# Kernel optimization log

Measured on AMD Instinct MI355X. Metric: run time of the kernel, lower is better.

The kernel has to match this reference:

```python
import jax, jax.numpy as jnp
import numpy as np

N, E, C = 20000, 320000, 10000
IN, H, D = 768, 8, 64
HD = H * D
SA_H = 128


def _gat(feat, src, dst, W, al, ar, b):
    # DGL GATConv: fc -> per-node attn terms -> edge leaky_relu -> edge softmax over dst -> scatter-add -> bias -> elu
    h = (feat @ W).reshape(N, H, D)                       # [N,H,D]
    el = (h * al).sum(-1)                                 # [N,H]
    er = (h * ar).sum(-1)                                 # [N,H]
    e = jax.nn.leaky_relu(el[src] + er[dst], 0.2)         # [E,H]
    m = jax.ops.segment_max(e, dst, num_segments=N)       # [N,H]
    m = jnp.where(jnp.isfinite(m), m, 0.0)                # zero in-degree nodes
    ee = jnp.exp(e - m[dst])                              # [E,H]
    denom = jax.ops.segment_sum(ee, dst, num_segments=N)  # [N,H]
    a = ee / jnp.maximum(denom[dst], 1e-9)                # [E,H]
    out = jax.ops.segment_sum(a[:, :, None] * h[src], dst, num_segments=N)  # [N,H,D]
    return jax.nn.elu(out + b.reshape(1, H, D))


def _sem(z, w1, b1, w2):
    # SemanticAttention: per-metapath score -> softmax over metapaths -> weighted sum
    w = (jnp.tanh(z @ w1 + b1) @ w2).mean(0)              # [M,1]
    beta = jax.nn.softmax(w, axis=0)                      # [M,1]
    return (beta[None] * z).sum(1)                        # [C,HD]


def setup_inputs():
    key = jax.random.key(0)
    ks = jax.random.split(key, 32)
    inp = {}
    for i in range(3):
        inp[f"feat{i}"] = jax.random.normal(ks[i], (N, IN), jnp.float32)
        inp[f"src{i}"] = jax.random.randint(ks[3 + i], (E,), 0, N, dtype=jnp.int32)
        inp[f"dst{i}"] = jax.random.randint(ks[6 + i], (E,), 0, N, dtype=jnp.int32)
        inp[f"char{i}"] = jnp.arange(C, dtype=jnp.int32)
        inp[f"W{i}"] = jax.random.normal(ks[9 + i], (IN, HD), jnp.float32) * 0.05
        inp[f"al{i}"] = jax.random.normal(ks[12 + i], (H, D), jnp.float32) * 0.05
        inp[f"ar{i}"] = jax.random.normal(ks[15 + i], (H, D), jnp.float32) * 0.05
        inp[f"b{i}"] = jnp.zeros((HD,), jnp.float32)
    inp["sw1"] = jax.random.normal(ks[18], (HD, SA_H), jnp.float32) * 0.05
    inp["sb1"] = jnp.zeros((SA_H,), jnp.float32)
    inp["sw2"] = jax.random.normal(ks[19], (SA_H, 1), jnp.float32) * 0.05
    inp["aw1"] = jax.random.normal(ks[20], (HD, SA_H), jnp.float32) * 0.05
    inp["ab1"] = jnp.zeros((SA_H,), jnp.float32)
    inp["aw2"] = jax.random.normal(ks[21], (SA_H, 1), jnp.float32) * 0.05
    return inp


def reference(feat0, feat1, feat2, src0, src1, src2, dst0, dst1, dst2, char0, char1, char2,
              W0, W1, W2, al0, al1, al2, ar0, ar1, ar2, b0, b1, b2,
              sw1, sb1, sw2, aw1, ab1, aw2):
    h1 = _gat(feat0, src0, dst0, W0, al0, ar0, b0)        # [N,H,D]
    hh = _gat(feat2, src2, dst2, W2, al2, ar2, b2)        # [N,H,D]
    z = jnp.stack([h1[char0].reshape(C, HD), hh[char2].reshape(C, HD)], axis=1)  # [C,2,HD]
    sound = _sem(z, sw1, sb1, sw2)                        # [C,HD]
    h2 = _gat(feat1, src1, dst1, W1, al1, ar1, b1)        # [N,H,D]
    z2 = jnp.stack([sound, h2[char1].reshape(C, HD)], axis=1)  # [C,2,HD]
    sem_emb = _sem(z2, aw1, ab1, aw2).reshape(C, H, D)    # [C,H,D]
    h1 = h1.at[char0].set(sem_emb)
    h2 = h2.at[char1].set(sem_emb)
    hh = hh.at[char2].set(sem_emb)
    return sem_emb, h1.mean(1), h2.mean(1), hh.mean(1)
```

## Files before the change

kernel.cpp:

```cpp
#include <hip/hip_runtime.h>
#include <math.h>

#define NN 20000
#define NE 320000
#define CC 10000
#define KIN 768
#define NH 8
#define ND 64
#define NHD 512
#define NSA 128
#define NBKT 79

#define WTB_SZ (NHD * KIN)
#define W1TB_SZ (NSA * NHD)

typedef __attribute__((ext_vector_type(4))) float f32x4;
typedef __attribute__((ext_vector_type(8))) short s16x8;

__device__ __forceinline__ unsigned short f2bf(float f) {
  unsigned u = __float_as_uint(f);
  u += 0x7fffu + ((u >> 16) & 1u);
  return (unsigned short)(u >> 16);
}
__device__ __forceinline__ float bf2f(unsigned short s) {
  return __uint_as_float(((unsigned)s) << 16);
}
__device__ __forceinline__ float bflo(unsigned u) { return __uint_as_float(u << 16); }
__device__ __forceinline__ float bfhi(unsigned u) { return __uint_as_float(u & 0xffff0000u); }

__device__ __forceinline__ void gl_lds16(const void* g, void* l) {
  __builtin_amdgcn_global_load_lds(
      (const __attribute__((address_space(1))) unsigned int*)g,
      (__attribute__((address_space(3))) unsigned int*)l, 16, 0, 0);
}

__global__ void k_prep(const float* __restrict__ W0, const float* __restrict__ W1,
                       const float* __restrict__ W2, const float* __restrict__ sw1,
                       const float* __restrict__ aw1, unsigned short* __restrict__ wtb3,
                       unsigned short* __restrict__ w1tb2, int* __restrict__ deg3,
                       float* __restrict__ scal) {
  int i = blockIdx.x * 256 + threadIdx.x;
  if (i < 3 * WTB_SZ) {
    int g = i / WTB_SZ;
    int j = i - g * WTB_SZ;
    int n = j / KIN, k = j - n * KIN;
    const float* W = (g == 0) ? W0 : (g == 1) ? W1 : W2;
    wtb3[i] = f2bf(W[(size_t)k * NHD + n]);
    return;
  }
  i -= 3 * WTB_SZ;
  if (i < 2 * W1TB_SZ) {
    int p = i / W1TB_SZ;
    int j = i - p * W1TB_SZ;
    int n = j / NHD, k = j - n * NHD;
    const float* W = p ? aw1 : sw1;
    w1tb2[p * W1TB_SZ + n * NHD + k] = f2bf(W[(size_t)k * NSA + n]);
    return;
  }
  i -= 2 * W1TB_SZ;
  if (i < 3 * NN) { deg3[i] = 0; return; }
  i -= 3 * NN;
  if (i < 4) scal[i] = 0.f;
}

__global__ __launch_bounds__(256, 2) void k_gemm_gat(const float* __restrict__ A,
                                                     const unsigned short* __restrict__ Bt,
                                                     unsigned short* __restrict__ outb,
                                                     const float* __restrict__ al,
                                                     const float* __restrict__ ar,
                                                     float* __restrict__ el,
                                                     float* __restrict__ er) {
  __shared__ unsigned short As[128 * 32];
  __shared__ unsigned short Bs[128 * 32];
  const int bid = blockIdx.x;
  const int xcd = bid & 7, t = bid >> 3;
  const int rowblk = (t >> 2) * 8 + xcd;
  if (rowblk * 128 >= NN) return;
  const int row0 = rowblk * 128;
  const int col0 = (t & 3) * 128;
  const int tid = threadIdx.x;
  const int wv = tid >> 6, lane = tid & 63;
  const int wr = (wv >> 1) * 64, wc = (wv & 1) * 64;
  const int ci = lane & 3, rsub = lane >> 2;

  f32x4 acc[4][4] = {};

  const int l15 = lane & 15;
  const int pc = (((lane >> 4) ^ ((l15 >> 1) & 3))) * 8;

  for (int k0 = 0; k0 < KIN; k0 += 32) {
#pragma unroll
    for (int i = 0; i < 2; i++) {
      int lrow = (wv * 2 + i) * 16 + rsub;
      int kc = (ci ^ ((lrow >> 1) & 3)) << 3;
      int ga = row0 + lrow; if (ga > NN - 1) ga = NN - 1;
      const float* ap = A + (size_t)ga * KIN + k0 + kc;
      float4 f0 = ((const float4*)ap)[0];
      float4 f1 = ((const float4*)ap)[1];
      int gb = col0 + lrow;
      gl_lds16(Bt + (size_t)gb * KIN + k0 + kc, Bs + (wv * 2 + i) * 512);
      uint4 pk;
      pk.x = ((unsigned)f2bf(f0.y) << 16) | f2bf(f0.x);
      pk.y = ((unsigned)f2bf(f0.w) << 16) | f2bf(f0.z);
      pk.z = ((unsigned)f2bf(f1.y) << 16) | f2bf(f1.x);
      pk.w = ((unsigned)f2bf(f1.w) << 16) | f2bf(f1.z);
      *(uint4*)(As + (wv * 2 + i) * 512 + lane * 8) = pk;
    }
    __syncthreads();
    s16x8 af[4], bf[4];
#pragma unroll
    for (int m = 0; m < 4; m++) {
      af[m] = *(const s16x8*)(As + (wr + m * 16 + l15) * 32 + pc);
      bf[m] = *(const s16x8*)(Bs + (wc + m * 16 + l15) * 32 + pc);
    }
#pragma unroll
    for (int m = 0; m < 4; m++)
#pragma unroll
      for (int n = 0; n < 4; n++)
        acc[m][n] = __builtin_amdgcn_mfma_f32_16x16x32_bf16(af[m], bf[n], acc[m][n], 0, 0, 0);
    __syncthreads();
  }

  const int cbase = col0 + wc + l15;
  const int rq = (lane >> 4) * 4;
  const int hd = (col0 + wc) >> 6;
  float alc[4], arc[4];
#pragma unroll
  for (int n = 0; n < 4; n++) { alc[n] = al[cbase + n * 16]; arc[n] = ar[cbase + n * 16]; }

#pragma unroll
  for (int m = 0; m < 4; m++) {
#pragma unroll
    for (int r = 0; r < 4; r++) {
      int grow = row0 + wr + m * 16 + rq + r;
      float a = 0.f, b = 0.f;
#pragma unroll
      for (int n = 0; n < 4; n++) {
        float v = acc[m][n][r];
        a += v * alc[n];
        b += v * arc[n];
      }
      a += __shfl_xor(a, 1, 64); a += __shfl_xor(a, 2, 64);
      a += __shfl_xor(a, 4, 64); a += __shfl_xor(a, 8, 64);
      b += __shfl_xor(b, 1, 64); b += __shfl_xor(b, 2, 64);
      b += __shfl_xor(b, 4, 64); b += __shfl_xor(b, 8, 64);
      if (grow < NN) {
        unsigned short* dp = outb + (size_t)grow * NHD + cbase;
#pragma unroll
        for (int n = 0; n < 4; n++) dp[n * 16] = f2bf(acc[m][n][r]);
        if (l15 == 0) {
          el[(size_t)grow * NH + hd] = a;
          er[(size_t)grow * NH + hd] = b;
        }
      }
    }
  }
}

__global__ __launch_bounds__(256, 2) void k_gemm_sem(const unsigned short* __restrict__ A0,
                                                     const unsigned short* __restrict__ A1,
                                                     const unsigned short* __restrict__ Bt,
                                                     const float* __restrict__ b1,
                                                     const float* __restrict__ w2,
                                                     float* __restrict__ scal) {
  __shared__ unsigned short As[128 * 32];
  __shared__ unsigned short Bs[128 * 32];
  __shared__ float rsum[2][128];
  __shared__ float pp[2][2];
  const int M = 2 * CC;
  const int tid = threadIdx.x;
  const int wv = tid >> 6, lane = tid & 63;
  const int row0 = blockIdx.x * 128;
  const int wr = (wv >> 1) * 64, wc = (wv & 1) * 64;
  const int ci = lane & 3, rsub = lane >> 2;

  f32x4 acc[4][4] = {};

  const int l15 = lane & 15;
  const int pc = (((lane >> 4) ^ ((l15 >> 1) & 3))) * 8;

  for (int k0 = 0; k0 < NHD; k0 += 32) {
#pragma unroll
    for (int i = 0; i < 2; i++) {
      int lrow = (wv * 2 + i) * 16 + rsub;
      int kc = (ci ^ ((lrow >> 1) & 3)) << 3;
      int ga = row0 + lrow; if (ga > M - 1) ga = M - 1;
      const unsigned short* Ap = (ga < CC) ? A0 + (size_t)ga * NHD
                                           : A1 + (size_t)(ga - CC) * NHD;
      gl_lds16(Ap + k0 + kc, As + (wv * 2 + i) * 512);
      int gb = lrow;
      gl_lds16(Bt + (size_t)gb * NHD + k0 + kc, Bs + (wv * 2 + i) * 512);
    }
    __syncthreads();
    s16x8 af[4], bf[4];
#pragma unroll
    for (int m = 0; m < 4; m++) {
      af[m] = *(const s16x8*)(As + (wr + m * 16 + l15) * 32 + pc);
      bf[m] = *(const s16x8*)(Bs + (wc + m * 16 + l15) * 32 + pc);
    }
#pragma unroll
    for (int m = 0; m < 4; m++)
#pragma unroll
      for (int n = 0; n < 4; n++)
        acc[m][n] = __builtin_amdgcn_mfma_f32_16x16x32_bf16(af[m], bf[n], acc[m][n], 0, 0, 0);
    __syncthreads();
  }

  if (tid < 128) { rsum[0][tid] = 0.f; rsum[1][tid] = 0.f; }
  __syncthreads();
  const int cb = wc + l15;
  const int rq = (lane >> 4) * 4;
  float b1c[4], w2c[4];
#pragma unroll
  for (int n = 0; n < 4; n++) { b1c[n] = b1[cb + n * 16]; w2c[n] = w2[cb + n * 16]; }
#pragma unroll
  for (int m = 0; m < 4; m++) {
#pragma unroll
    for (int r = 0; r < 4; r++) {
      int rl = wr + m * 16 + rq + r;
      float s = 0.f;
#pragma unroll
      for (int n = 0; n < 4; n++) s += tanhf(acc[m][n][r] + b1c[n]) * w2c[n];
      s += __shfl_xor(s, 1, 64); s += __shfl_xor(s, 2, 64);
      s += __shfl_xor(s, 4, 64); s += __shfl_xor(s, 8, 64);
      if (l15 == 0 && row0 + rl < M) rsum[wv & 1][rl] = s;
    }
  }
  __syncthreads();
  if (tid < 128) {
    int grow = row0 + tid;
    float v = rsum[0][tid] + rsum[1][tid];
    float vA = (grow < CC) ? v : 0.f;
    float vB = (grow >= CC && grow < M) ? v : 0.f;
#pragma unroll
    for (int off = 32; off > 0; off >>= 1) {
      vA += __shfl_xor(vA, off, 64);
      vB += __shfl_xor(vB, off, 64);
    }
    if ((tid & 63) == 0) { pp[tid >> 6][0] = vA; pp[tid >> 6][1] = vB; }
  }
  __syncthreads();
  if (tid == 0) {
    atomicAdd(scal + 0, pp[0][0] + pp[1][0]);
    atomicAdd(scal + 1, pp[0][1] + pp[1][1]);
  }
}

__global__ void k_hist3(const int* __restrict__ d0, const int* __restrict__ d1,
                        const int* __restrict__ d2, int* __restrict__ deg3) {
  int e = blockIdx.x * 256 + threadIdx.x;
  int g = blockIdx.y;
  const int* dst = (g == 0) ? d0 : (g == 1) ? d1 : d2;
  atomicAdd(deg3 + g * NN + dst[e], 1);
}

__global__ __launch_bounds__(1024) void k_scan3(const int* __restrict__ deg3,
                                                int* __restrict__ rowptr3,
                                                int* __restrict__ curB) {
  __shared__ int part[1024];
  const int g = blockIdx.x;
  const int* deg = deg3 + g * NN;
  int* rowptr = rowptr3 + g * (NN + 1);
  int tid = threadIdx.x;
  const int CH = 20;
  int base = tid * CH;
  int s = 0;
  for (int i = 0; i < CH; i++) { int idx = base + i; if (idx < NN) s += deg[idx]; }
  part[tid] = s;
  __syncthreads();
  for (int off = 1; off < 1024; off <<= 1) {
    int u = (tid >= off) ? part[tid - off] : 0;
    int v = part[tid];
    __syncthreads();
    part[tid] = u + v;
    __syncthreads();
  }
  int run = (tid == 0) ? 0 : part[tid - 1];
  for (int i = 0; i < CH; i++) {
    int idx = base + i;
    if (idx < NN) {
      rowptr[idx] = run;
      if ((idx & 255) == 0) curB[g * (NBKT + 1) + (idx >> 8)] = run;
      run += deg[idx];
    }
  }
  if (tid == 1023) rowptr[NN] = part[1023];
}

__global__ __launch_bounds__(1024) void k_coarse(const int* __restrict__ s0,
                                                 const int* __restrict__ s1,
                                                 const int* __restrict__ s2,
                                                 const int* __restrict__ d0,
                                                 const int* __restrict__ d1,
                                                 const int* __restrict__ d2,
                                                 int* __restrict__ curB,
                                                 unsigned* __restrict__ staging) {
  __shared__ int bcnt[NBKT];
  __shared__ int bbase[NBKT];
  int g = blockIdx.y;
  const int* src = (g == 0) ? s0 : (g == 1) ? s1 : s2;
  const int* dst = (g == 0) ? d0 : (g == 1) ? d1 : d2;
  int tid = threadIdx.x;
  if (tid < NBKT) bcnt[tid] = 0;
  __syncthreads();
  int e = blockIdx.x * 1024 + tid;
  bool val = e < NE;
  int b = 0, r = 0, sv = 0, dv = 0;
  if (val) {
    dv = dst[e]; sv = src[e];
    b = dv >> 8;
    r = atomicAdd(&bcnt[b], 1);
  }
  __syncthreads();
  if (tid < NBKT && bcnt[tid] > 0) bbase[tid] = atomicAdd(&curB[g * (NBKT + 1) + tid], bcnt[tid]);
  __syncthreads();
  if (val) staging[(size_t)g * NE + bbase[b] + r] = ((unsigned)sv << 8) | (unsigned)(dv & 255);
}

__global__ __launch_bounds__(1024) void k_fine(const int* __restrict__ rowptr3,
                                               const unsigned* __restrict__ staging,
                                               unsigned short* __restrict__ srcord3) {
  __shared__ int cur[256];
  int g = blockIdx.y, b = blockIdx.x;
  const int* rowptr = rowptr3 + g * (NN + 1);
  int n0 = b << 8;
  int tid = threadIdx.x;
  if (tid < 256) {
    int node = n0 + tid;
    cur[tid] = (node < NN) ? rowptr[node] : 0;
  }
  __syncthreads();
  int nend = n0 + 256; if (nend > NN) nend = NN;
  int start = rowptr[n0];
  int endp = rowptr[nend];
  for (int i = start + tid; i < endp; i += 1024) {
    unsigned u = staging[(size_t)g * NE + i];
    int nl = u & 255;
    int pos = atomicAdd(&cur[nl], 1);
    srcord3[(size_t)g * NE + pos] = (unsigned short)(u >> 8);
  }
}

__global__ __launch_bounds__(256) void k_aggf(const int* __restrict__ rowptr,
                                              const unsigned short* __restrict__ srcord,
                                              const float* __restrict__ el,
                                              const float* __restrict__ er,
                                              const unsigned short* __restrict__ hb,
                                              const float* __restrict__ bias,
                                              unsigned short* __restrict__ ob) {
  __shared__ float aS[4][64 * 8];
  __shared__ int sS[4][64];
  int wv = threadIdx.x >> 6;
  int t = (blockIdx.x * 256 + threadIdx.x) >> 6;
  int lane = threadIdx.x & 63;
  int h = lane >> 3;
  int beg = rowptr[t], end = rowptr[t + 1];

  float4 er0 = ((const float4*)(er + (size_t)t * NH))[0];
  float4 er1 = ((const float4*)(er + (size_t)t * NH))[1];
  float erow[8] = {er0.x, er0.y, er0.z, er0.w, er1.x, er1.y, er1.z, er1.w};

  float acc[8] = {0.f, 0.f, 0.f, 0.f, 0.f, 0.f, 0.f, 0.f};
  float den = 0.f;

  for (int cbeg = beg; cbeg < end; cbeg += 64) {
    int cnt = end - cbeg; if (cnt > 64) cnt = 64;
    bool valid = lane < cnt;
    int pidx = cbeg + lane; if (pidx > end - 1) pidx = end - 1;
    int s = srcord[pidx];
    if (valid) {
      sS[wv][lane] = s;
      float4 a0 = ((const float4*)(el + (size_t)s * NH))[0];
      float4 a1 = ((const float4*)(el + (size_t)s * NH))[1];
      float v[8] = {a0.x + erow[0], a0.y + erow[1], a0.z + erow[2], a0.w + erow[3],
                    a1.x + erow[4], a1.y + erow[5], a1.z + erow[6], a1.w + erow[7]};
#pragma unroll
      for (int k = 0; k < 8; k++) {
        float x = v[k];
        x = x >= 0.f ? x : 0.2f * x;
        aS[wv][lane * 8 + k] = __expf(x);
      }
    }
    const unsigned short* hbl = hb + lane * 8;
    int q = 0;
    for (; q + 3 < cnt; q += 4) {
      int s0 = sS[wv][q], s1 = sS[wv][q + 1], s2 = sS[wv][q + 2], s3 = sS[wv][q + 3];
      float w0 = aS[wv][q * 8 + h];
      float w1 = aS[wv][(q + 1) * 8 + h];
      float w2 = aS[wv][(q + 2) * 8 + h];
      float w3 = aS[wv][(q + 3) * 8 + h];
      uint4 v0 = *(const uint4*)(hbl + (size_t)s0 * NHD);
      uint4 v1 = *(const uint4*)(hbl + (size_t)s1 * NHD);
      uint4 v2 = *(const uint4*)(hbl + (size_t)s2 * NHD);
      uint4 v3 = *(const uint4*)(hbl + (size_t)s3 * NHD);
      den += (w0 + w1) + (w2 + w3);
      acc[0] += w0 * bflo(v0.x); acc[1] += w0 * bfhi(v0.x);
      acc[2] += w0 * bflo(v0.y); acc[3] += w0 * bfhi(v0.y);
      acc[4] += w0 * bflo(v0.z); acc[5] += w0 * bfhi(v0.z);
      acc[6] += w0 * bflo(v0.w); acc[7] += w0 * bfhi(v0.w);
      acc[0] += w1 * bflo(v1.x); acc[1] += w1 * bfhi(v1.x);
      acc[2] += w1 * bflo(v1.y); acc[3] += w1 * bfhi(v1.y);
      acc[4] += w1 * bflo(v1.z); acc[5] += w1 * bfhi(v1.z);
      acc[6] += w1 * bflo(v1.w); acc[7] += w1 * bfhi(v1.w);
      acc[0] += w2 * bflo(v2.x); acc[1] += w2 * bfhi(v2.x);
      acc[2] += w2 * bflo(v2.y); acc[3] += w2 * bfhi(v2.y);
      acc[4] += w2 * bflo(v2.z); acc[5] += w2 * bfhi(v2.z);
      acc[6] += w2 * bflo(v2.w); acc[7] += w2 * bfhi(v2.w);
      acc[0] += w3 * bflo(v3.x); acc[1] += w3 * bfhi(v3.x);
      acc[2] += w3 * bflo(v3.y); acc[3] += w3 * bfhi(v3.y);
      acc[4] += w3 * bflo(v3.z); acc[5] += w3 * bfhi(v3.z);
      acc[6] += w3 * bflo(v3.w); acc[7] += w3 * bfhi(v3.w);
    }
    for (; q < cnt; q++) {
      int s0 = sS[wv][q];
      float w0 = aS[wv][q * 8 + h];
      uint4 v0 = *(const uint4*)(hbl + (size_t)s0 * NHD);
      den += w0;
      acc[0] += w0 * bflo(v0.x); acc[1] += w0 * bfhi(v0.x);
      acc[2] += w0 * bflo(v0.y); acc[3] += w0 * bfhi(v0.y);
      acc[4] += w0 * bflo(v0.z); acc[5] += w0 * bfhi(v0.z);
      acc[6] += w0 * bflo(v0.w); acc[7] += w0 * bfhi(v0.w);
    }
  }

  float dn = 1.f / fmaxf(den, 1e-9f);
  float4 b0 = ((const float4*)(bias + lane * 8))[0];
  float4 b1 = ((const float4*)(bias + lane * 8))[1];
  float r[8];
  r[0] = acc[0] * dn + b0.x; r[1] = acc[1] * dn + b0.y;
  r[2] = acc[2] * dn + b0.z; r[3] = acc[3] * dn + b0.w;
  r[4] = acc[4] * dn + b1.x; r[5] = acc[5] * dn + b1.y;
  r[6] = acc[6] * dn + b1.z; r[7] = acc[7] * dn + b1.w;
#pragma unroll
  for (int j = 0; j < 8; j++) r[j] = r[j] > 0.f ? r[j] : expm1f(r[j]);
  uint4 z;
  z.x = ((unsigned)f2bf(r[1]) << 16) | f2bf(r[0]);
  z.y = ((unsigned)f2bf(r[3]) << 16) | f2bf(r[2]);
  z.z = ((unsigned)f2bf(r[5]) << 16) | f2bf(r[4]);
  z.w = ((unsigned)f2bf(r[7]) << 16) | f2bf(r[6]);
  *(uint4*)(ob + (size_t)t * NHD + lane * 8) = z;
}

__global__ void k_combine_s1(const float* __restrict__ scal,
                             const unsigned short* __restrict__ zA,
                             const unsigned short* __restrict__ zB,
                             unsigned short* __restrict__ outb) {
  int i = blockIdx.x * 256 + threadIdx.x;
  float w0 = scal[0] * (1.f / CC), w1v = scal[1] * (1.f / CC);
  float mx = fmaxf(w0, w1v);
  float e0 = expf(w0 - mx), e1 = expf(w1v - mx);
  float inv = 1.f / (e0 + e1);
  float b0 = e0 * inv, b1v = e1 * inv;
  ushort4 a = ((const ushort4*)zA)[i];
  ushort4 b = ((const ushort4*)zB)[i];
  ushort4 z;
  z.x = f2bf(b0 * bf2f(a.x) + b1v * bf2f(b.x));
  z.y = f2bf(b0 * bf2f(a.y) + b1v * bf2f(b.y));
  z.z = f2bf(b0 * bf2f(a.z) + b1v * bf2f(b.z));
  z.w = f2bf(b0 * bf2f(a.w) + b1v * bf2f(b.w));
  ((ushort4*)outb)[i] = z;
}

__global__ void k_comb2_means(const float* __restrict__ scal,
                              const unsigned short* __restrict__ zsound,
                              const unsigned short* __restrict__ ob0,
                              const unsigned short* __restrict__ ob1,
                              const unsigned short* __restrict__ ob2,
                              float* __restrict__ outf,
                              float* __restrict__ m1, float* __restrict__ m2,
                              float* __restrict__ m3) {
  int idx = blockIdx.x * 256 + threadIdx.x;
  int n = idx >> 6, d = idx & 63;
  if (n < CC) {
    float w0 = scal[0] * (1.f / CC), w1v = scal[1] * (1.f / CC);
    float mx = fmaxf(w0, w1v);
    float e0 = expf(w0 - mx), e1 = expf(w1v - mx);
    float inv = 1.f / (e0 + e1);
    float b0 = e0 * inv, b1v = e1 * inv;
    const unsigned short* zs = zsound + (size_t)n * NHD + d;
    const unsigned short* p1 = ob1 + (size_t)n * NHD + d;
    float* po = outf + (size_t)n * NHD + d;
    float v = 0.f;
#pragma unroll
    for (int h = 0; h < 8; h++) {
      float r = b0 * bf2f(zs[h * 64]) + b1v * bf2f(p1[h * 64]);
      po[h * 64] = r;
      v += r;
    }
    v *= 0.125f;
    m1[idx] = v; m2[idx] = v; m3[idx] = v;
  } else {
    const unsigned short* p0 = ob0 + (size_t)n * NHD + d;
    const unsigned short* p1 = ob1 + (size_t)n * NHD + d;
    const unsigned short* p2 = ob2 + (size_t)n * NHD + d;
    float v0 = 0.f, v1 = 0.f, v2 = 0.f;
#pragma unroll
    for (int h = 0; h < 8; h++) {
      v0 += bf2f(p0[h * 64]); v1 += bf2f(p1[h * 64]); v2 += bf2f(p2[h * 64]);
    }
    m1[idx] = v0 * 0.125f; m2[idx] = v1 * 0.125f; m3[idx] = v2 * 0.125f;
  }
}

extern "C" void kernel_launch(void* const* d_in, const int* in_sizes, int n_in,
                              void* d_out, int out_size, void* d_ws, size_t ws_size,
                              hipStream_t stream) {
  (void)in_sizes; (void)n_in; (void)out_size; (void)ws_size;

  const float* feat[3]; const int* srcp[3]; const int* dstp[3];
  const float* Wp[3]; const float* alp[3]; const float* arp[3]; const float* bp[3];
  for (int g = 0; g < 3; g++) {
    const int base = g * 8;
    feat[g] = (const float*)d_in[base + 0];
    srcp[g] = (const int*)d_in[base + 1];
    dstp[g] = (const int*)d_in[base + 2];
    Wp[g]   = (const float*)d_in[base + 4];
    alp[g]  = (const float*)d_in[base + 5];
    arp[g]  = (const float*)d_in[base + 6];
    bp[g]   = (const float*)d_in[base + 7];
  }
  const float* sw1 = (const float*)d_in[24];
  const float* sb1 = (const float*)d_in[25];
  const float* sw2 = (const float*)d_in[26];
  const float* aw1 = (const float*)d_in[27];
  const float* ab1 = (const float*)d_in[28];
  const float* aw2 = (const float*)d_in[29];

  char* wsp = (char*)d_ws;
  auto alloc = [&](size_t bytes) {
    char* p = wsp;
    wsp += (bytes + 255) & ~(size_t)255;
    return p;
  };
  unsigned short* ob0 = (unsigned short*)alloc((size_t)NN * NHD * 2);
  unsigned short* ob1 = (unsigned short*)alloc((size_t)NN * NHD * 2);
  unsigned short* ob2 = (unsigned short*)alloc((size_t)NN * NHD * 2);
  unsigned short* hb = (unsigned short*)alloc((size_t)NN * NHD * 2);
  unsigned short* wtb3 = (unsigned short*)alloc((size_t)3 * WTB_SZ * 2);
  unsigned short* w1tb2 = (unsigned short*)alloc((size_t)2 * W1TB_SZ * 2);
  unsigned short* sound = (unsigned short*)alloc((size_t)CC * NHD * 2);
  float* el = (float*)alloc((size_t)NN * NH * 4);
  float* er = (float*)alloc((size_t)NN * NH * 4);
  float* scal = (float*)alloc(256);
  int* deg3 = (int*)alloc((size_t)3 * NN * 4);
  int* rowptr3 = (int*)alloc((size_t)3 * (NN + 1) * 4 + 64);
  int* curB = (int*)alloc((size_t)3 * (NBKT + 1) * 4);
  unsigned* staging = (unsigned*)alloc((size_t)3 * NE * 4);
  unsigned short* srcord3 = (unsigned short*)alloc((size_t)3 * NE * 2);

  float* outf = (float*)d_out;
  float* outm1 = outf + (size_t)CC * NHD;
  float* outm2 = outm1 + (size_t)NN * ND;
  float* outm3 = outm2 + (size_t)NN * ND;

  const int PREP_T = 3 * WTB_SZ + 2 * W1TB_SZ + 3 * NN + 4;
  k_prep<<<(PREP_T + 255) / 256, 256, 0, stream>>>(Wp[0], Wp[1], Wp[2], sw1, aw1,
                                                   wtb3, w1tb2, deg3, scal);
  k_hist3<<<dim3(NE / 256, 3), 256, 0, stream>>>(dstp[0], dstp[1], dstp[2], deg3);
  k_scan3<<<3, 1024, 0, stream>>>(deg3, rowptr3, curB);
  k_coarse<<<dim3((NE + 1023) / 1024, 3), 1024, 0, stream>>>(
      srcp[0], srcp[1], srcp[2], dstp[0], dstp[1], dstp[2], curB, staging);
  k_fine<<<dim3(NBKT, 3), 1024, 0, stream>>>(rowptr3, staging, srcord3);

  auto gat = [&](int g, unsigned short* ob) {
    k_gemm_gat<<<640, 256, 0, stream>>>(
        feat[g], wtb3 + (size_t)g * WTB_SZ, hb, alp[g], arp[g], el, er);
    k_aggf<<<NN * 64 / 256, 256, 0, stream>>>(rowptr3 + g * (NN + 1), srcord3 + (size_t)g * NE,
                                              el, er, hb, bp[g], ob);
  };

  gat(0, ob0);
  gat(2, ob2);

  k_gemm_sem<<<(2 * CC + 127) / 128, 256, 0, stream>>>(ob0, ob2, w1tb2, sb1, sw2, scal);
  k_combine_s1<<<CC * NHD / 4 / 256, 256, 0, stream>>>(scal, ob0, ob2, sound);

  gat(1, ob1);

  k_gemm_sem<<<(2 * CC + 127) / 128, 256, 0, stream>>>(sound, ob1, w1tb2 + W1TB_SZ, ab1, aw2, scal + 2);
  k_comb2_means<<<NN * 64 / 256, 256, 0, stream>>>(scal + 2, sound, ob0, ob1, ob2,
                                                   outf, outm1, outm2, outm3);
}
```

Before: 451.0 us.

## Double-buffer LDS and register-prefetch two K-steps ahead in GAT GEMM

The projection GEMM now keeps two LDS buffers for A and B and prefetches global tiles into registers two K-steps ahead, which removes the second barrier per iteration. The B operand no longer uses the direct global-to-LDS load and instead goes through registers. The goal is to hide global load latency behind the MFMA work. The cost is more register pressure under launch_bounds(256,2) and twice the shared memory.

```diff
diff --git a/kernel.cpp b/kernel.cpp
--- a/kernel.cpp
+++ b/kernel.cpp
@@ -70,8 +70,8 @@
                                                      const float* __restrict__ ar,
                                                      float* __restrict__ el,
                                                      float* __restrict__ er) {
-  __shared__ unsigned short As[128 * 32];
-  __shared__ unsigned short Bs[128 * 32];
+  __shared__ unsigned short As[2][128 * 32];
+  __shared__ unsigned short Bs[2][128 * 32];
   const int bid = blockIdx.x;
   const int xcd = bid & 7, t = bid >> 3;
   const int rowblk = (t >> 2) * 8 + xcd;
@@ -88,37 +88,68 @@
   const int l15 = lane & 15;
   const int pc = (((lane >> 4) ^ ((l15 >> 1) & 3))) * 8;
 
-  for (int k0 = 0; k0 < KIN; k0 += 32) {
+  const float* aptr[2];
+  const unsigned short* bptr[2];
+  int ldsoff[2];
+#pragma unroll
+  for (int i = 0; i < 2; i++) {
+    int lrow = (wv * 2 + i) * 16 + rsub;
+    int kc = (ci ^ ((lrow >> 1) & 3)) << 3;
+    int ga = row0 + lrow; if (ga > NN - 1) ga = NN - 1;
+    aptr[i] = A + (size_t)ga * KIN + kc;
+    bptr[i] = Bt + (size_t)(col0 + lrow) * KIN + kc;
+    ldsoff[i] = (wv * 2 + i) * 512 + lane * 8;
+  }
+
+  const int NSTEP = KIN / 32;
+  float4 fa[2][2][2];
+  uint4 bb[2][2];
+
+#pragma unroll
+  for (int s = 0; s < 2; s++)
 #pragma unroll
     for (int i = 0; i < 2; i++) {
-      int lrow = (wv * 2 + i) * 16 + rsub;
-      int kc = (ci ^ ((lrow >> 1) & 3)) << 3;
-      int ga = row0 + lrow; if (ga > NN - 1) ga = NN - 1;
-      const float* ap = A + (size_t)ga * KIN + k0 + kc;
-      float4 f0 = ((const float4*)ap)[0];
-      float4 f1 = ((const float4*)ap)[1];
-      int gb = col0 + lrow;
-      gl_lds16(Bt + (size_t)gb * KIN + k0 + kc, Bs + (wv * 2 + i) * 512);
+      fa[s][i][0] = ((const float4*)(aptr[i] + s * 32))[0];
+      fa[s][i][1] = ((const float4*)(aptr[i] + s * 32))[1];
+      bb[s][i] = *(const uint4*)(bptr[i] + s * 32);
+    }
+
+  int cur = 0;
+  for (int ks = 0; ks < NSTEP; ks++) {
+    int p = ks & 1;
+#pragma unroll
+    for (int i = 0; i < 2; i++) {
+      float4 f0 = fa[p][i][0], f1 = fa[p][i][1];
       uint4 pk;
       pk.x = ((unsigned)f2bf(f0.y) << 16) | f2bf(f0.x);
       pk.y = ((unsigned)f2bf(f0.w) << 16) | f2bf(f0.z);
       pk.z = ((unsigned)f2bf(f1.y) << 16) | f2bf(f1.x);
       pk.w = ((unsigned)f2bf(f1.w) << 16) | f2bf(f1.z);
-      *(uint4*)(As + (wv * 2 + i) * 512 + lane * 8) = pk;
+      *(uint4*)(As[cur] + ldsoff[i]) = pk;
+      *(uint4*)(Bs[cur] + ldsoff[i]) = bb[p][i];
+    }
+    if (ks + 2 < NSTEP) {
+      int k0n = (ks + 2) * 32;
+#pragma unroll
+      for (int i = 0; i < 2; i++) {
+        fa[p][i][0] = ((const float4*)(aptr[i] + k0n))[0];
+        fa[p][i][1] = ((const float4*)(aptr[i] + k0n))[1];
+        bb[p][i] = *(const uint4*)(bptr[i] + k0n);
+      }
     }
     __syncthreads();
     s16x8 af[4], bf[4];
 #pragma unroll
     for (int m = 0; m < 4; m++) {
-      af[m] = *(const s16x8*)(As + (wr + m * 16 + l15) * 32 + pc);
-      bf[m] = *(const s16x8*)(Bs + (wc + m * 16 + l15) * 32 + pc);
+      af[m] = *(const s16x8*)(As[cur] + (wr + m * 16 + l15) * 32 + pc);
+      bf[m] = *(const s16x8*)(Bs[cur] + (wc + m * 16 + l15) * 32 + pc);
     }
 #pragma unroll
     for (int m = 0; m < 4; m++)
 #pragma unroll
       for (int n = 0; n < 4; n++)
         acc[m][n] = __builtin_amdgcn_mfma_f32_16x16x32_bf16(af[m], bf[n], acc[m][n], 0, 0, 0);
-    __syncthreads();
+    cur ^= 1;
   }
 
   const int cbase = col0 + wc + l15;
```

Result: slower. 884.7 us (+96.2%).

## Double-buffer GAT GEMM LDS tiles with register prefetch two steps ahead

Applied to the files above, without the earlier changes.

The GAT projection GEMM now uses two LDS buffers for both A and B. Global loads for the next k-steps are issued into registers two steps ahead, and B is now loaded through registers instead of the direct global-to-LDS load. The aim is to overlap global memory latency with MFMA work and cut the barriers to one per k-step. The trade-off is higher register use from the prefetch buffers and twice the LDS, which may reduce occupancy.

```diff
diff --git a/kernel.cpp b/kernel.cpp
--- a/kernel.cpp
+++ b/kernel.cpp
@@ -32,6 +32,15 @@
   __builtin_amdgcn_global_load_lds(
       (const __attribute__((address_space(1))) unsigned int*)g,
       (__attribute__((address_space(3))) unsigned int*)l, 16, 0, 0);
+}
+
+__device__ __forceinline__ uint4 packbf(float4 f0, float4 f1) {
+  uint4 pk;
+  pk.x = ((unsigned)f2bf(f0.y) << 16) | f2bf(f0.x);
+  pk.y = ((unsigned)f2bf(f0.w) << 16) | f2bf(f0.z);
+  pk.z = ((unsigned)f2bf(f1.y) << 16) | f2bf(f1.x);
+  pk.w = ((unsigned)f2bf(f1.w) << 16) | f2bf(f1.z);
+  return pk;
 }
 
 __global__ void k_prep(const float* __restrict__ W0, const float* __restrict__ W1,
@@ -70,8 +79,8 @@
                                                      const float* __restrict__ ar,
                                                      float* __restrict__ el,
                                                      float* __restrict__ er) {
-  __shared__ unsigned short As[128 * 32];
-  __shared__ unsigned short Bs[128 * 32];
+  __shared__ unsigned short As[2][128 * 32];
+  __shared__ unsigned short Bs[2][128 * 32];
   const int bid = blockIdx.x;
   const int xcd = bid & 7, t = bid >> 3;
   const int rowblk = (t >> 2) * 8 + xcd;
@@ -88,38 +97,82 @@
   const int l15 = lane & 15;
   const int pc = (((lane >> 4) ^ ((l15 >> 1) & 3))) * 8;
 
-  for (int k0 = 0; k0 < KIN; k0 += 32) {
-#pragma unroll
-    for (int i = 0; i < 2; i++) {
-      int lrow = (wv * 2 + i) * 16 + rsub;
-      int kc = (ci ^ ((lrow >> 1) & 3)) << 3;
-      int ga = row0 + lrow; if (ga > NN - 1) ga = NN - 1;
-      const float* ap = A + (size_t)ga * KIN + k0 + kc;
-      float4 f0 = ((const float4*)ap)[0];
-      float4 f1 = ((const float4*)ap)[1];
-      int gb = col0 + lrow;
-      gl_lds16(Bt + (size_t)gb * KIN + k0 + kc, Bs + (wv * 2 + i) * 512);
-      uint4 pk;
-      pk.x = ((unsigned)f2bf(f0.y) << 16) | f2bf(f0.x);
-      pk.y = ((unsigned)f2bf(f0.w) << 16) | f2bf(f0.z);
-      pk.z = ((unsigned)f2bf(f1.y) << 16) | f2bf(f1.x);
-      pk.w = ((unsigned)f2bf(f1.w) << 16) | f2bf(f1.z);
-      *(uint4*)(As + (wv * 2 + i) * 512 + lane * 8) = pk;
+  const float* ap0; const float* ap1;
+  const unsigned short* bp0; const unsigned short* bp1;
+  int lo0, lo1;
+  {
+    int lrow = (wv * 2 + 0) * 16 + rsub;
+    int kc = (ci ^ ((lrow >> 1) & 3)) << 3;
+    int ga = row0 + lrow; if (ga > NN - 1) ga = NN - 1;
+    ap0 = A + (size_t)ga * KIN + kc;
+    bp0 = Bt + (size_t)(col0 + lrow) * KIN + kc;
+    lo0 = (wv * 2 + 0) * 512 + lane * 8;
+  }
+  {
+    int lrow = (wv * 2 + 1) * 16 + rsub;
+    int kc = (ci ^ ((lrow >> 1) & 3)) << 3;
+    int ga = row0 + lrow; if (ga > NN - 1) ga = NN - 1;
+    ap1 = A + (size_t)ga * KIN + kc;
+    bp1 = Bt + (size_t)(col0 + lrow) * KIN + kc;
+    lo1 = (wv * 2 + 1) * 512 + lane * 8;
+  }
+
+  const int NSTEP = KIN / 32;
+
+  float4 s0a0, s0a1, s0a2, s0a3;  uint4 s0b0, s0b1;
+  float4 s1a0, s1a1, s1a2, s1a3;  uint4 s1b0, s1b1;
+
+  s0a0 = ((const float4*)(ap0 + 0))[0];  s0a1 = ((const float4*)(ap0 + 0))[1];
+  s0a2 = ((const float4*)(ap1 + 0))[0];  s0a3 = ((const float4*)(ap1 + 0))[1];
+  s0b0 = *(const uint4*)(bp0 + 0);       s0b1 = *(const uint4*)(bp1 + 0);
+  s1a0 = ((const float4*)(ap0 + 32))[0]; s1a1 = ((const float4*)(ap0 + 32))[1];
+  s1a2 = ((const float4*)(ap1 + 32))[0]; s1a3 = ((const float4*)(ap1 + 32))[1];
+  s1b0 = *(const uint4*)(bp0 + 32);      s1b1 = *(const uint4*)(bp1 + 32);
+
+#define MFMA_PHASE(BUF)                                                          \
+  {                                                                              \
+    s16x8 af[4], bf[4];                                                          \
+    _Pragma("unroll")                                                            \
+    for (int m = 0; m < 4; m++) {                                                \
+      af[m] = *(const s16x8*)(As[BUF] + (wr + m * 16 + l15) * 32 + pc);          \
+      bf[m] = *(const s16x8*)(Bs[BUF] + (wc + m * 16 + l15) * 32 + pc);          \
+    }                                                                            \
+    _Pragma("unroll")                                                            \
+    for (int m = 0; m < 4; m++)                                                  \
+      _Pragma("unroll")                                                          \
+      for (int n = 0; n < 4; n++)                                                \
+        acc[m][n] = __builtin_amdgcn_mfma_f32_16x16x32_bf16(af[m], bf[n],        \
+                                                            acc[m][n], 0, 0, 0); \
+  }
+
+  for (int ks = 0; ks < NSTEP; ks += 2) {
+    *(uint4*)(As[0] + lo0) = packbf(s0a0, s0a1);
+    *(uint4*)(As[0] + lo1) = packbf(s0a2, s0a3);
+    *(uint4*)(Bs[0] + lo0) = s0b0;
+    *(uint4*)(Bs[0] + lo1) = s0b1;
+    if (ks + 2 < NSTEP) {
+      int k0n = (ks + 2) * 32;
+      s0a0 = ((const float4*)(ap0 + k0n))[0];  s0a1 = ((const float4*)(ap0 + k0n))[1];
+      s0a2 = ((const float4*)(ap1 + k0n))[0];  s0a3 = ((const float4*)(ap1 + k0n))[1];
+      s0b0 = *(const uint4*)(bp0 + k0n);       s0b1 = *(const uint4*)(bp1 + k0n);
     }
     __syncthreads();
-    s16x8 af[4], bf[4];
-#pragma unroll
-    for (int m = 0; m < 4; m++) {
-      af[m] = *(const s16x8*)(As + (wr + m * 16 + l15) * 32 + pc);
-      bf[m] = *(const s16x8*)(Bs + (wc + m * 16 + l15) * 32 + pc);
-    }
-#pragma unroll
-    for (int m = 0; m < 4; m++)
-#pragma unroll
-      for (int n = 0; n < 4; n++)
-        acc[m][n] = __builtin_amdgcn_mfma_f32_16x16x32_bf16(af[m], bf[n], acc[m][n], 0, 0, 0);
+    MFMA_PHASE(0)
+
+    *(uint4*)(As[1] + lo0) = packbf(s1a0, s1a1);
+    *(uint4*)(As[1] + lo1) = packbf(s1a2, s1a3);
+    *(uint4*)(Bs[1] + lo0) = s1b0;
+    *(uint4*)(Bs[1] + lo1) = s1b1;
+    if (ks + 3 < NSTEP) {
+      int k0n = (ks + 3) * 32;
+      s1a0 = ((const float4*)(ap0 + k0n))[0];  s1a1 = ((const float4*)(ap0 + k0n))[1];
+      s1a2 = ((const float4*)(ap1 + k0n))[0];  s1a3 = ((const float4*)(ap1 + k0n))[1];
+      s1b0 = *(const uint4*)(bp0 + k0n);       s1b1 = *(const uint4*)(bp1 + k0n);
+    }
     __syncthreads();
-  }
+    MFMA_PHASE(1)
+  }
+#undef MFMA_PHASE
 
   const int cbase = col0 + wc + l15;
   const int rq = (lane >> 4) * 4;
```

After: 457.2 us. Within noise of the previous version (+1.4%).
